# Kernel tuning notes

Hardware: AMD Instinct MI355X
Metric: run time of the kernel (lower is better)

Reference implementation:

```python
import jax, jax.numpy as jnp
import numpy as np

MAX_DISP = 2  # 5x5x5 = 125 shifts


def conv3d(x, w, b):
    # x: [N,C,D,H,W], w: [O,I,3,3,3], padding 1 == SAME for stride 1
    y = jax.lax.conv_general_dilated(x, w, (1, 1, 1), 'SAME',
                                     dimension_numbers=('NCDHW', 'OIDHW', 'NCDHW'))
    return y + b[None, :, None, None, None]


def _warp_one(vol, flw):
    # vol: [C,H,W,D], flw: [3,H,W,D]; trilinear sampling at grid+flow, border-clamped
    C, H, W, D = vol.shape
    gz, gy, gx = jnp.meshgrid(jnp.arange(H, dtype=jnp.float32),
                              jnp.arange(W, dtype=jnp.float32),
                              jnp.arange(D, dtype=jnp.float32), indexing='ij')
    z = gz + flw[0]; y = gy + flw[1]; x = gx + flw[2]
    z0f, y0f, x0f = jnp.floor(z), jnp.floor(y), jnp.floor(x)
    wz, wy, wx = z - z0f, y - y0f, x - x0f
    z0 = jnp.clip(z0f, 0, H - 1).astype(jnp.int32)
    z1 = jnp.clip(z0f + 1, 0, H - 1).astype(jnp.int32)
    y0 = jnp.clip(y0f, 0, W - 1).astype(jnp.int32)
    y1 = jnp.clip(y0f + 1, 0, W - 1).astype(jnp.int32)
    x0 = jnp.clip(x0f, 0, D - 1).astype(jnp.int32)
    x1 = jnp.clip(x0f + 1, 0, D - 1).astype(jnp.int32)
    out = jnp.zeros_like(vol)
    for zi, wzi in ((z0, 1.0 - wz), (z1, wz)):
        for yi, wyi in ((y0, 1.0 - wy), (y1, wy)):
            for xi, wxi in ((x0, 1.0 - wx), (x1, wx)):
                out = out + vol[:, zi, yi, xi] * (wzi * wyi * wxi)[None]
    return out


warp = jax.vmap(_warp_one)


def compute_cost_volume(f1, f2, max_disp):
    B, C, H, W, D = f1.shape
    f2p = jnp.pad(f2, ((0, 0), (0, 0), (max_disp, max_disp), (max_disp, max_disp), (max_disp, max_disp)))
    n = 2 * max_disp + 1
    cost = []
    for i in range(n):
        for j in range(n):
            for k in range(n):
                cost.append(jnp.mean(f1 * f2p[:, :, i:H + i, j:W + j, k:D + k], axis=1, keepdims=True))
    return jnp.concatenate(cost, axis=1)  # [B,125,H,W,D]


def reference(moving, fixed, flow, context, w0, b0, w1, b1, w2, b2, w3, b3, w4, b4):
    shape = moving.shape[2:]
    up_context = jax.image.resize(context, context.shape[:2] + shape, method='trilinear')
    warped = warp(moving, flow)
    # normalize_features(normalize=True, center=True, across_channels=True, across_images=True)
    axes = (1, 2, 3, 4)
    m = 0.5 * (jnp.mean(warped, axes, keepdims=True) + jnp.mean(fixed, axes, keepdims=True))
    s = 0.5 * (jnp.std(warped, axis=axes, ddof=1, keepdims=True) +
               jnp.std(fixed, axis=axes, ddof=1, keepdims=True))
    warped_n = (warped - m) / s
    fixed_n = (fixed - m) / s
    cv = jax.nn.leaky_relu(compute_cost_volume(fixed_n, warped_n, MAX_DISP), 0.05)
    x_in = jnp.concatenate([up_context, flow, cv, fixed], axis=1)  # 32+3+125+16 = 176 ch
    ws = [w0, w1, w2, w3]
    bs = [b0, b1, b2, b3]
    x_out = x_in
    for w, b in zip(ws, bs):
        x_out = jax.nn.leaky_relu(conv3d(x_in, w, b), 0.02)
        x_in = jnp.concatenate([x_in, x_out], axis=1)
    context_out = x_out
    refinement = conv3d(context_out, w4, b4)
    return context_out, flow + refinement


def setup_inputs() -> dict:
    key = jax.random.key(0)
    ks = jax.random.split(key, 16)
    B, C, S = 1, 16, 48
    inp = {
        'moving': jax.random.normal(ks[0], (B, C, S, S, S), jnp.float32),
        'fixed': jax.random.normal(ks[1], (B, C, S, S, S), jnp.float32),
        'flow': jax.random.normal(ks[2], (B, 3, S, S, S), jnp.float32),
        'context': jax.random.normal(ks[3], (B, 32, S // 2, S // 2, S // 2), jnp.float32),
    }
    chans_in = [176, 240, 288, 320, 16]
    chans_out = [64, 48, 32, 16, 3]
    for i, (ci, co) in enumerate(zip(chans_in, chans_out)):
        inp[f'w{i}'] = 0.02 * jax.random.normal(ks[4 + i], (co, ci, 3, 3, 3), jnp.float32)
        inp[f'b{i}'] = jnp.zeros((co,), jnp.float32)
    return inp
```

## Files before the change

kernel.cpp:

```cpp
#include <hip/hip_runtime.h>
#include <cstddef>

#define SD 48
#define VOX (SD*SD*SD)
#define CSD 24
#define CVOL (CSD*CSD*CSD)
#define CST 352
#define PPL 2500
#define XPBYTES 88000000ull

typedef __attribute__((ext_vector_type(8))) short short8v;
typedef __attribute__((ext_vector_type(4))) short short4v;
typedef __attribute__((ext_vector_type(4))) float float4v;

__device__ __forceinline__ float lrelu(float x, float a){ return x > 0.f ? x : a*x; }

__device__ __forceinline__ unsigned short f2bf(float f){
    unsigned u = __float_as_uint(f);
    unsigned r = (u + 0x7fffu + ((u >> 16) & 1u)) >> 16;
    return (unsigned short)r;
}
__device__ __forceinline__ float bf2f(unsigned short s){
    return __uint_as_float(((unsigned)s) << 16);
}
__device__ __forceinline__ unsigned pk2(float a, float b){
    return (unsigned)f2bf(a) | ((unsigned)f2bf(b) << 16);
}

__device__ __forceinline__ void decode(int v, int &i, int &j, int &k){
    i = v / (SD*SD);
    int r = v - i*(SD*SD);
    j = r / SD;
    k = r - j*SD;
}

__global__ __launch_bounds__(256) void k_warp_prep(
        const float* __restrict__ moving, const float* __restrict__ fixd,
        const float* __restrict__ flow, const float* __restrict__ context,
        unsigned short* __restrict__ WARPB, float* __restrict__ part,
        unsigned short* __restrict__ Xp)
{
    if (blockIdx.x >= 432){
        int v = (blockIdx.x - 432)*256 + threadIdx.x;
        if (v < 125000){
            int pz = v / 2500, r = v % 2500, py = r / 50, px = r % 50;
            if (pz==0||pz==49||py==0||py==49||px==0||px==49){
                uint4* p = (uint4*)(Xp + (size_t)v*CST);
                uint4 zz = make_uint4(0,0,0,0);
                #pragma unroll
                for (int g=0; g<44; g++) p[g] = zz;
            }
        }
        return;
    }
    int v = blockIdx.x*256 + threadIdx.x;
    int i,j,k; decode(v,i,j,k);
    size_t pvox = (size_t)((i+1)*PPL + (j+1)*50 + (k+1))*CST;

    float f0 = flow[v], f1 = flow[VOX+v], f2v = flow[2*VOX+v];
    float z = (float)i + f0;
    float y = (float)j + f1;
    float x = (float)k + f2v;
    float z0f=floorf(z), y0f=floorf(y), x0f=floorf(x);
    float wz=z-z0f, wy=y-y0f, wx=x-x0f;
    int z0=min(max((int)z0f,0),SD-1), z1=min(max((int)z0f+1,0),SD-1);
    int y0=min(max((int)y0f,0),SD-1), y1=min(max((int)y0f+1,0),SD-1);
    int x0=min(max((int)x0f,0),SD-1), x1=min(max((int)x0f+1,0),SD-1);
    int b000=(z0*SD+y0)*SD+x0, b001=(z0*SD+y0)*SD+x1;
    int b010=(z0*SD+y1)*SD+x0, b011=(z0*SD+y1)*SD+x1;
    int b100=(z1*SD+y0)*SD+x0, b101=(z1*SD+y0)*SD+x1;
    int b110=(z1*SD+y1)*SD+x0, b111=(z1*SD+y1)*SD+x1;
    float w000=(1.f-wz)*(1.f-wy)*(1.f-wx), w001=(1.f-wz)*(1.f-wy)*wx;
    float w010=(1.f-wz)*wy*(1.f-wx),       w011=(1.f-wz)*wy*wx;
    float w100=wz*(1.f-wy)*(1.f-wx),       w101=wz*(1.f-wy)*wx;
    float w110=wz*wy*(1.f-wx),             w111=wz*wy*wx;

    float ow[16];
    float sw=0.f, ssw=0.f, sf=0.f, ssf=0.f;
    #pragma unroll
    for (int c=0;c<16;c++){
        const float* mc = moving + (size_t)c*VOX;
        float o = mc[b000]*w000 + mc[b001]*w001 + mc[b010]*w010 + mc[b011]*w011
                + mc[b100]*w100 + mc[b101]*w101 + mc[b110]*w110 + mc[b111]*w111;
        ow[c] = o;
        sw += o; ssw += o*o;
        float f = fixd[(size_t)c*VOX+v];
        sf += f; ssf += f*f;
    }
    uint4 q0 = make_uint4(pk2(ow[0],ow[1]), pk2(ow[2],ow[3]), pk2(ow[4],ow[5]), pk2(ow[6],ow[7]));
    uint4 q1 = make_uint4(pk2(ow[8],ow[9]), pk2(ow[10],ow[11]), pk2(ow[12],ow[13]), pk2(ow[14],ow[15]));
    uint4* wp = (uint4*)(WARPB + (size_t)v*16);
    wp[0] = q0; wp[1] = q1;

    float zc=0.5f*(float)i-0.25f, yc=0.5f*(float)j-0.25f, xc=0.5f*(float)k-0.25f;
    float cz0f=floorf(zc), cy0f=floorf(yc), cx0f=floorf(xc);
    float cwz=zc-cz0f, cwy=yc-cy0f, cwx=xc-cx0f;
    int cz0=min(max((int)cz0f,0),CSD-1), cz1=min(max((int)cz0f+1,0),CSD-1);
    int cy0=min(max((int)cy0f,0),CSD-1), cy1=min(max((int)cy0f+1,0),CSD-1);
    int cx0=min(max((int)cx0f,0),CSD-1), cx1=min(max((int)cx0f+1,0),CSD-1);
    int c000=(cz0*CSD+cy0)*CSD+cx0, c001=(cz0*CSD+cy0)*CSD+cx1;
    int c010=(cz0*CSD+cy1)*CSD+cx0, c011=(cz0*CSD+cy1)*CSD+cx1;
    int c100=(cz1*CSD+cy0)*CSD+cx0, c101=(cz1*CSD+cy0)*CSD+cx1;
    int c110=(cz1*CSD+cy1)*CSD+cx0, c111=(cz1*CSD+cy1)*CSD+cx1;
    float u000=(1.f-cwz)*(1.f-cwy)*(1.f-cwx), u001=(1.f-cwz)*(1.f-cwy)*cwx;
    float u010=(1.f-cwz)*cwy*(1.f-cwx),       u011=(1.f-cwz)*cwy*cwx;
    float u100=cwz*(1.f-cwy)*(1.f-cwx),       u101=cwz*(1.f-cwy)*cwx;
    float u110=cwz*cwy*(1.f-cwx),             u111=cwz*cwy*cwx;

    float oc[32];
    #pragma unroll
    for (int c=0;c<32;c++){
        const float* cc = context + (size_t)c*CVOL;
        oc[c] = cc[c000]*u000 + cc[c001]*u001 + cc[c010]*u010 + cc[c011]*u011
              + cc[c100]*u100 + cc[c101]*u101 + cc[c110]*u110 + cc[c111]*u111;
    }
    uint4* dst = (uint4*)(Xp + pvox);
    #pragma unroll
    for (int g=0; g<4; g++)
        dst[g] = make_uint4(pk2(oc[g*8+0],oc[g*8+1]), pk2(oc[g*8+2],oc[g*8+3]),
                            pk2(oc[g*8+4],oc[g*8+5]), pk2(oc[g*8+6],oc[g*8+7]));
    *(unsigned*)(Xp + pvox + 32) = pk2(f0, f1);
    Xp[pvox + 34] = f2bf(f2v);
    float fx[16];
    #pragma unroll
    for (int c=0;c<16;c++) fx[c] = fixd[(size_t)c*VOX+v];
    uint4* dstF = (uint4*)(Xp + pvox + 160);
    dstF[0] = make_uint4(pk2(fx[0],fx[1]),  pk2(fx[2],fx[3]),  pk2(fx[4],fx[5]),  pk2(fx[6],fx[7]));
    dstF[1] = make_uint4(pk2(fx[8],fx[9]),  pk2(fx[10],fx[11]),pk2(fx[12],fx[13]),pk2(fx[14],fx[15]));

    __shared__ float4 red[256];
    int tid=threadIdx.x;
    red[tid] = make_float4(sw,ssw,sf,ssf);
    __syncthreads();
    for (int off=128; off>0; off>>=1){
        if (tid<off){
            float4 a=red[tid], b2=red[tid+off];
            red[tid]=make_float4(a.x+b2.x, a.y+b2.y, a.z+b2.z, a.w+b2.w);
        }
        __syncthreads();
    }
    if (tid==0){
        float4 r=red[0];
        part[blockIdx.x]       = r.x;
        part[432+blockIdx.x]   = r.y;
        part[864+blockIdx.x]   = r.z;
        part[1296+blockIdx.x]  = r.w;
    }
}

__global__ __launch_bounds__(256) void k_stats(const float* __restrict__ part,
                                               float* __restrict__ stats)
{
    int tid=threadIdx.x;
    double acc[4]={0,0,0,0};
    for (int i=tid;i<432;i+=256){
        acc[0]+=part[i]; acc[1]+=part[432+i]; acc[2]+=part[864+i]; acc[3]+=part[1296+i];
    }
    __shared__ double red[256];
    double res[4]={0,0,0,0};
    for (int q=0;q<4;q++){
        red[tid]=acc[q]; __syncthreads();
        for (int off=128;off>0;off>>=1){
            if (tid<off) red[tid]+=red[tid+off];
            __syncthreads();
        }
        res[q]=red[0];
        __syncthreads();
    }
    if (tid==0){
        double N = 16.0*(double)VOX;
        double mw = res[0]/N, mf = res[2]/N;
        double vw = (res[1] - res[0]*res[0]/N)/(N-1.0);
        double vf = (res[3] - res[2]*res[2]/N)/(N-1.0);
        double m = 0.5*(mw+mf);
        double s = 0.5*(sqrt(vw)+sqrt(vf));
        stats[0]=(float)m;
        stats[1]=(float)(1.0/s);
    }
}

__global__ __launch_bounds__(256) void k_cv(
        const float* __restrict__ fixd, const unsigned short* __restrict__ WARPB,
        const float* __restrict__ stats, unsigned short* __restrict__ Xp)
{
    int v = blockIdx.x*256 + threadIdx.x;
    int i,j,k; decode(v,i,j,k);
    size_t pvox = (size_t)((i+1)*PPL + (j+1)*50 + (k+1))*CST;
    float m = stats[0], inv_s = stats[1];
    float fn[16]; float sfn = 0.f;
    #pragma unroll
    for (int c=0;c<16;c++){ fn[c] = (fixd[(size_t)c*VOX+v]-m)*inv_s; sfn += fn[c]; }
    float scale = inv_s*(1.0f/16.0f);
    float msfn = m*sfn;

    float res[125];
    #pragma unroll
    for (int dz=-2;dz<=2;dz++){
        int zz=i+dz;
        #pragma unroll
        for (int dy=-2;dy<=2;dy++){
            int yy=j+dy;
            #pragma unroll
            for (int dx=-2;dx<=2;dx++){
                int xx=k+dx;
                const int r = (dz+2)*25+(dy+2)*5+(dx+2);
                float o = 0.f;
                if ((unsigned)zz<SD && (unsigned)yy<SD && (unsigned)xx<SD){
                    int vs=(zz*SD+yy)*SD+xx;
                    const short8v* wr = (const short8v*)(WARPB + (size_t)vs*16);
                    short8v wlo = wr[0], whi = wr[1];
                    float d = 0.f;
                    #pragma unroll
                    for (int e=0;e<8;e++) d += fn[e]   * bf2f((unsigned short)wlo[e]);
                    #pragma unroll
                    for (int e=0;e<8;e++) d += fn[8+e] * bf2f((unsigned short)whi[e]);
                    o = lrelu(scale*(d - msfn), 0.05f);
                }
                res[r] = o;
            }
        }
    }
    Xp[pvox + 35] = f2bf(res[0]);
    {
        short4v s4;
        #pragma unroll
        for (int e=0;e<4;e++) s4[e] = (short)f2bf(res[1+e]);
        *(short4v*)(Xp + pvox + 36) = s4;
    }
    #pragma unroll
    for (int g=0; g<15; g++){
        short8v s8;
        #pragma unroll
        for (int e=0;e<8;e++) s8[e] = (short)f2bf(res[5+g*8+e]);
        *(short8v*)(Xp + pvox + 40 + g*8) = s8;
    }
}

__device__ __forceinline__ void wb_one(int idx, const float* __restrict__ w,
        unsigned short* __restrict__ dst, int CO, int CIN, int CT)
{
    int e = idx & 7;
    int l = (idx >> 3) & 63;
    int rest = idx >> 9;
    int ct = rest % CT;
    int rest2 = rest / CT;
    int tn = rest2 % 27;
    int chunk = rest2 / 27;
    int dz = tn/9, rr = tn%9, dxx = rr/3, dyy = rr%3;
    int t_orig = dz*9 + dyy*3 + dxx;
    int co = ct*16 + (l & 15);
    int cin = chunk*32 + (l >> 4)*8 + e;
    unsigned short v = 0;
    if (co < CO && cin < CIN) v = f2bf(w[((size_t)co*CIN + cin)*27 + t_orig]);
    dst[idx] = v;
}

__global__ __launch_bounds__(256) void k_wb_all(
        const float* __restrict__ w0, const float* __restrict__ w1,
        const float* __restrict__ w2, const float* __restrict__ w3,
        const float* __restrict__ w4,
        unsigned short* __restrict__ Wb0, unsigned short* __restrict__ Wb1,
        unsigned short* __restrict__ Wb2, unsigned short* __restrict__ Wb3,
        unsigned short* __restrict__ Wb4)
{
    const int n0=331776, n1=331776, n2=248832, n3=138240, n4=13824;
    int idx = blockIdx.x*256 + threadIdx.x;
    if (idx < n0){ wb_one(idx, w0, Wb0, 64, 176, 4); return; }
    idx -= n0;
    if (idx < n1){ wb_one(idx, w1, Wb1, 48, 240, 3); return; }
    idx -= n1;
    if (idx < n2){ wb_one(idx, w2, Wb2, 32, 288, 2); return; }
    idx -= n2;
    if (idx < n3){ wb_one(idx, w3, Wb3, 16, 320, 1); return; }
    idx -= n3;
    if (idx < n4){ wb_one(idx, w4, Wb4,  3,  16, 1); return; }
}

template<int CT, int DEPTH, int MODE>
__global__ __launch_bounds__(128) void k_mconv(
        const unsigned short* __restrict__ Xp,
        const unsigned short* __restrict__ Wb,
        const float* __restrict__ bias,
        int nchunks, int ch_base,
        unsigned short* __restrict__ Ydst,
        float* __restrict__ outf,
        const float* __restrict__ flw)
{
    __shared__ unsigned short slab[13824];
    const int tid = threadIdx.x;
    const int bid0 = blockIdx.x;
    const int bid = (bid0 & 7)*108 + (bid0 >> 3);
    const int xt = bid % 3, yt = (bid/3) % 12, zt = bid / 36;
    const int x0 = xt*16, y0 = yt*4, z0 = zt*2;
    const int lane = tid & 63, w = tid >> 6;
    const int lx = lane & 15, kb = lane >> 4;

    int voff[14];
    #pragma unroll
    for (int i=0;i<14;i++){
        int u = tid + i*128;
        int p = u >> 2, q = u & 3;
        int sx = p % 18; int pr = p / 18; int sy = pr % 6; int sz = pr / 6;
        sz = min(sz, 3);
        voff[i] = ((z0+sz)*PPL + (y0+sy)*50 + (x0+sx))*CST + q*8;
    }

    float4v acc[4][CT];
    #pragma unroll
    for (int vt=0; vt<4; vt++)
        #pragma unroll
        for (int ct=0; ct<CT; ct++)
            acc[vt][ct] = (float4v){0.f,0.f,0.f,0.f};

    const unsigned short* wl = Wb + (size_t)lane*8;
    const int gmax = nchunks*27 - 1;
    short8v a[DEPTH][CT];
    #pragma unroll
    for (int d=0; d<DEPTH-1; d++)
        #pragma unroll
        for (int ct=0; ct<CT; ct++)
            a[d][ct] = *(const short8v*)(wl + (size_t)min(d,gmax)*(CT*512) + (size_t)ct*512);

    for (int chunk=0; chunk<nchunks; chunk++){
        const int cb = ch_base + chunk*32;
        __syncthreads();
        #pragma unroll
        for (int i=0;i<14;i++){
            int u = tid + i*128;
            if (i < 13 || u < 1728){
                const unsigned short* g = Xp + voff[i] + cb;
                __builtin_amdgcn_global_load_lds(
                    (const __attribute__((address_space(1))) void*)g,
                    (__attribute__((address_space(3))) void*)(slab + (size_t)u*8),
                    16, 0, 0);
            }
        }
        __syncthreads();

        const int gb = chunk*27;
        #pragma unroll
        for (int dz=0; dz<3; dz++){
            #pragma unroll
            for (int dxx=0; dxx<3; dxx++){
                short8v brow[6];
                #pragma unroll
                for (int yi=0; yi<6; yi++)
                    brow[yi] = *(const short8v*)(slab
                        + (size_t)((((w+dz)*6 + yi)*18 + dxx + lx)*32 + kb*8));
                #pragma unroll
                for (int dyy=0; dyy<3; dyy++){
                    const int t = dz*9 + dxx*3 + dyy;
                    {
                        int g2 = gb + t + (DEPTH-1); g2 = min(g2, gmax);
                        #pragma unroll
                        for (int ct=0; ct<CT; ct++)
                            a[(t+DEPTH-1)%DEPTH][ct] = *(const short8v*)(wl
                                + (size_t)g2*(CT*512) + (size_t)ct*512);
                    }
                    __builtin_amdgcn_s_setprio(1);
                    #pragma unroll
                    for (int vt=0; vt<4; vt++)
                        #pragma unroll
                        for (int ct=0; ct<CT; ct++)
                            acc[vt][ct] = __builtin_amdgcn_mfma_f32_16x16x32_bf16(
                                              a[t%DEPTH][ct], brow[vt+dyy], acc[vt][ct], 0, 0, 0);
                    __builtin_amdgcn_s_setprio(0);
                }
            }
        }
    }

    const int x = x0 + lx, z = z0 + w;
    #pragma unroll
    for (int vt=0; vt<4; vt++){
        const int y = y0 + vt;
        const size_t pvox = (size_t)((z+1)*PPL + (y+1)*50 + (x+1))*CST;
        const int vi = (z*SD + y)*SD + x;
        #pragma unroll
        for (int ct=0; ct<CT; ct++){
            if (MODE == 2){
                #pragma unroll
                for (int r=0; r<4; r++){
                    const int co = ct*16 + kb*4 + r;
                    if (co < 3){
                        float vv = acc[vt][ct][r] + bias[co];
                        outf[(size_t)co*VOX + vi] = flw[(size_t)co*VOX + vi] + vv;
                    }
                }
            } else {
                const int co0 = ct*16 + kb*4;
                short4v s4;
                #pragma unroll
                for (int r=0; r<4; r++){
                    float vv = acc[vt][ct][r] + bias[co0+r];
                    float o = lrelu(vv, 0.02f);
                    s4[r] = (short)f2bf(o);
                    if (MODE == 1)
                        outf[(size_t)(co0+r)*VOX + vi] = o;
                }
                *(short4v*)(Ydst + pvox + co0) = s4;
            }
        }
    }
}

extern "C" void kernel_launch(void* const* d_in, const int* in_sizes, int n_in,
                              void* d_out, int out_size, void* d_ws, size_t ws_size,
                              hipStream_t stream) {
    const float* moving  = (const float*)d_in[0];
    const float* fixd    = (const float*)d_in[1];
    const float* flow    = (const float*)d_in[2];
    const float* context = (const float*)d_in[3];
    const float* w0 = (const float*)d_in[4];  const float* b0 = (const float*)d_in[5];
    const float* w1 = (const float*)d_in[6];  const float* b1 = (const float*)d_in[7];
    const float* w2 = (const float*)d_in[8];  const float* b2 = (const float*)d_in[9];
    const float* w3 = (const float*)d_in[10]; const float* b3 = (const float*)d_in[11];
    const float* w4 = (const float*)d_in[12]; const float* b4 = (const float*)d_in[13];

    char* ws = (char*)d_ws;
    unsigned short* Xp    = (unsigned short*)ws;
    unsigned short* WARPB = (unsigned short*)(ws + XPBYTES);
    float* PART  = (float*)(ws + XPBYTES + 3538944ull);
    float* STATS = (float*)(ws + XPBYTES + 3538944ull + 8192ull);
    unsigned short* Wb0 = (unsigned short*)(ws + XPBYTES + 3538944ull + 9216ull);
    unsigned short* Wb1 = Wb0 + (size_t)331776;
    unsigned short* Wb2 = Wb1 + (size_t)331776;
    unsigned short* Wb3 = Wb2 + (size_t)248832;
    unsigned short* Wb4 = Wb3 + (size_t)138240;

    float* ctx_out  = (float*)d_out;
    float* flow_out = (float*)d_out + (size_t)16*VOX;

    k_warp_prep<<<921,256,0,stream>>>(moving, fixd, flow, context, WARPB, PART, Xp);
    k_stats<<<1,256,0,stream>>>(PART, STATS);
    k_cv<<<432,256,0,stream>>>(fixd, WARPB, STATS, Xp);
    k_wb_all<<<4158,256,0,stream>>>(w0, w1, w2, w3, w4, Wb0, Wb1, Wb2, Wb3, Wb4);

    k_mconv<4,3,0><<<864,128,0,stream>>>(Xp, Wb0, b0, 6,  0,   Xp+176, nullptr, nullptr);
    k_mconv<3,3,0><<<864,128,0,stream>>>(Xp, Wb1, b1, 8,  0,   Xp+240, nullptr, nullptr);
    k_mconv<2,9,0><<<864,128,0,stream>>>(Xp, Wb2, b2, 9,  0,   Xp+288, nullptr, nullptr);
    k_mconv<1,9,1><<<864,128,0,stream>>>(Xp, Wb3, b3, 10, 0,   Xp+320, ctx_out, nullptr);
    k_mconv<1,3,2><<<864,128,0,stream>>>(Xp, Wb4, b4, 1,  320, Xp,     flow_out, flow);
}
```

Baseline: 383.1 us.

## Prefetch next channel chunk into registers while computing current chunk

Replaces the direct global-to-LDS loads of each 32-channel input slab with a register-staged software pipeline. The next chunk's slab is loaded into 14 uint4 registers per thread while the MFMA loop runs on the current slab, then written to LDS between barriers. This hides global load latency behind compute, at the cost of about 56 extra VGPRs per thread, which may reduce occupancy or cause spills alongside the accumulator and weight prefetch registers.

```diff
diff --git a/kernel.cpp b/kernel.cpp
--- a/kernel.cpp
+++ b/kernel.cpp
@@ -321,21 +321,35 @@
         for (int ct=0; ct<CT; ct++)
             a[d][ct] = *(const short8v*)(wl + (size_t)min(d,gmax)*(CT*512) + (size_t)ct*512);
 
-    for (int chunk=0; chunk<nchunks; chunk++){
-        const int cb = ch_base + chunk*32;
-        __syncthreads();
+    uint4 st[14];
+
+    {
+        const int cb = ch_base;
         #pragma unroll
         for (int i=0;i<14;i++){
             int u = tid + i*128;
-            if (i < 13 || u < 1728){
-                const unsigned short* g = Xp + voff[i] + cb;
-                __builtin_amdgcn_global_load_lds(
-                    (const __attribute__((address_space(1))) void*)g,
-                    (__attribute__((address_space(3))) void*)(slab + (size_t)u*8),
-                    16, 0, 0);
-            }
+            if (i < 13 || u < 1728)
+                st[i] = *(const uint4*)(Xp + voff[i] + cb);
+        }
+        #pragma unroll
+        for (int i=0;i<14;i++){
+            int u = tid + i*128;
+            if (i < 13 || u < 1728)
+                *(uint4*)(slab + (size_t)u*8) = st[i];
         }
         __syncthreads();
+    }
+
+    for (int chunk=0; chunk<nchunks; chunk++){
+        if (chunk+1 < nchunks){
+            const int cb = ch_base + (chunk+1)*32;
+            #pragma unroll
+            for (int i=0;i<14;i++){
+                int u = tid + i*128;
+                if (i < 13 || u < 1728)
+                    st[i] = *(const uint4*)(Xp + voff[i] + cb);
+            }
+        }
 
         const int gb = chunk*27;
         #pragma unroll
@@ -368,6 +382,17 @@
                 }
             }
         }
+
+        if (chunk+1 < nchunks){
+            __syncthreads();
+            #pragma unroll
+            for (int i=0;i<14;i++){
+                int u = tid + i*128;
+                if (i < 13 || u < 1728)
+                    *(uint4*)(slab + (size_t)u*8) = st[i];
+            }
+            __syncthreads();
+        }
     }
 
     const int x = x0 + lx, z = z0 + w;
```

New measurement: 603.5 us. 1.58x slower.
